# Kernel tuning notes

Hardware: AMD Instinct MI355X
Metric: run time of the kernel (lower is better)

## Reference

```python
import jax, jax.numpy as jnp
import numpy as np

B, S, H, F, K = 32, 512, 256, 256, 3
NBINS, MAX_MEL = 256, 2048


def _conv1d(x, w, b):
    # x: [B,S,Cin], w: [K,Cin,Cout] -> [B,S,Cout], padding 1 (SAME, k=3)
    return jax.lax.conv_general_dilated(x, w, (1,), 'SAME',
        dimension_numbers=('NWC', 'WIO', 'NWC')) + b


def _ln(x, g, b):
    m = jnp.mean(x, -1, keepdims=True)
    v = jnp.var(x, -1, keepdims=True)
    return (x - m) * jax.lax.rsqrt(v + 1e-5) * g + b


def _predictor(x, mask, p):
    # FastSpeech2 VariancePredictor (eval mode, dropout off)
    w1, b1, g1, be1, w2, b2, g2, be2, wl, bl = p
    h = _ln(jax.nn.relu(_conv1d(x, w1, b1)), g1, be1)
    h = _ln(jax.nn.relu(_conv1d(h, w2, b2)), g2, be2)
    out = (h @ wl + bl)[..., 0]  # [B,S]
    return jnp.where(mask, 0.0, out)  # masked_fill(mask, 0.0)


def _make_predictor_params(key, out_bias):
    ks = jax.random.split(key, 3)
    w1 = jax.random.normal(ks[0], (K, H, F), jnp.float32) * 0.03
    w2 = jax.random.normal(ks[1], (K, F, F), jnp.float32) * 0.03
    wl = jax.random.normal(ks[2], (F, 1), jnp.float32) * 0.02
    return [w1, jnp.zeros((F,), jnp.float32), jnp.ones((F,), jnp.float32), jnp.zeros((F,), jnp.float32),
            w2, jnp.zeros((F,), jnp.float32), jnp.ones((F,), jnp.float32), jnp.zeros((F,), jnp.float32),
            wl, jnp.full((1,), out_bias, jnp.float32)]


PNAMES = ['w1', 'b1', 'g1', 'be1', 'w2', 'b2', 'g2', 'be2', 'wl', 'bl']


def setup_inputs() -> dict:
    key = jax.random.key(0)
    ks = jax.random.split(key, 8)
    inp = {
        'x': jax.random.normal(ks[0], (B, S, H), jnp.float32),
        'src_mask': jnp.zeros((B, S), jnp.bool_),  # True = padded position
        'pitch_control': jnp.float32(1.0),
        'energy_control': jnp.float32(1.0),
        'duration_control': jnp.float32(1.0),
        'pitch_bins': jnp.linspace(-4.0, 4.0, NBINS - 1, dtype=jnp.float32),
        'energy_bins': jnp.linspace(-4.0, 4.0, NBINS - 1, dtype=jnp.float32),
        'pitch_emb': jax.random.normal(ks[1], (NBINS, H), jnp.float32) * 0.02,
        'energy_emb': jax.random.normal(ks[2], (NBINS, H), jnp.float32) * 0.02,
    }
    # duration predictor output bias 1.6 ~ log(5) -> avg ~4 frames/phoneme
    for i, (pref, ob) in enumerate([('dur', 1.6), ('pit', 0.0), ('ene', 0.0)]):
        for n, v in zip(PNAMES, _make_predictor_params(ks[3 + i], ob)):
            inp[pref + '_' + n] = v
    return inp


def reference(x, src_mask, pitch_control, energy_control, duration_control,
              pitch_bins, energy_bins, pitch_emb, energy_emb,
              dur_w1, dur_b1, dur_g1, dur_be1, dur_w2, dur_b2, dur_g2, dur_be2, dur_wl, dur_bl,
              pit_w1, pit_b1, pit_g1, pit_be1, pit_w2, pit_b2, pit_g2, pit_be2, pit_wl, pit_bl,
              ene_w1, ene_b1, ene_g1, ene_be1, ene_w2, ene_b2, ene_g2, ene_be2, ene_wl, ene_bl):
    dur_p = [dur_w1, dur_b1, dur_g1, dur_be1, dur_w2, dur_b2, dur_g2, dur_be2, dur_wl, dur_bl]
    pit_p = [pit_w1, pit_b1, pit_g1, pit_be1, pit_w2, pit_b2, pit_g2, pit_be2, pit_wl, pit_bl]
    ene_p = [ene_w1, ene_b1, ene_g1, ene_be1, ene_w2, ene_b2, ene_g2, ene_be2, ene_wl, ene_bl]

    log_dur = _predictor(x, src_mask, dur_p)                      # [B,S]
    pitch_pred = _predictor(x, src_mask, pit_p) * pitch_control   # inference: scaled prediction
    # torch.bucketize(v, bins) (right=False) == searchsorted side='left'
    x = x + pitch_emb[jnp.searchsorted(pitch_bins, pitch_pred, side='left')]
    energy_pred = _predictor(x, src_mask, ene_p) * energy_control
    x = x + energy_emb[jnp.searchsorted(energy_bins, energy_pred, side='left')]

    dur = jnp.maximum(jnp.round(jnp.exp(log_dur) - 1.0) * duration_control, 0.0)  # [B,S]
    dur_i = dur.astype(jnp.int32)
    mel_len = jnp.minimum(jnp.sum(dur_i, -1), MAX_MEL)            # [B]
    # Length regulator: frame t maps to phoneme idx = #{cumdur <= t}
    cum = jnp.cumsum(dur_i, 1)                                    # [B,S]
    t = jnp.arange(MAX_MEL, dtype=jnp.int32)
    idx = jax.vmap(lambda c: jnp.searchsorted(c, t, side='right'))(cum)  # [B,MAX_MEL]
    idx = jnp.clip(idx, 0, S - 1)
    x_exp = jnp.take_along_axis(x, idx[:, :, None], axis=1)       # [B,MAX_MEL,H]
    mel_mask = t[None, :] >= mel_len[:, None]                     # True = padded frame
    x_exp = jnp.where(mel_mask[:, :, None], 0.0, x_exp)
    return (x_exp, pitch_pred, energy_pred, log_dur, dur, mel_len, mel_mask)
```

## Files before the change

### kernel.cpp

```cpp
#include <hip/hip_runtime.h>
#include <stdint.h>

#define BB 32
#define SS 512
#define HH 256
#define MM (BB*SS)
#define MAXMEL 2048

typedef _Float16 f16;
typedef _Float16 f16x4 __attribute__((ext_vector_type(4)));
typedef _Float16 f16x8 __attribute__((ext_vector_type(8)));
typedef float    f32x16 __attribute__((ext_vector_type(16)));

#define BAR()  asm volatile("s_barrier" ::: "memory")
#define VMW9() asm volatile("s_waitcnt vmcnt(9)" ::: "memory")
#define VMW0() asm volatile("s_waitcnt vmcnt(0)" ::: "memory")

__device__ __forceinline__ size_t xoff(int row, int chan) {
  return ((size_t)(chan >> 4) * MM + row) * 16 + (chan & 15);
}

#define AOFF  49152
#define ABUF  12352
#define AZ    61440
#define BBUF  24576
#define LDSSZ 73856
#define WSZP ((size_t)393216)

template<int NS, int RAW>
__global__ __launch_bounds__(256) void conv16(
    const f16* __restrict__ X0h, const f16* __restrict__ X0l,
    const f16* __restrict__ X1h_, const f16* __restrict__ X1l_,
    const f16* __restrict__ W0, const f16* __restrict__ W1,
    const float* __restrict__ bias0, const float* __restrict__ bias1,
    f16* __restrict__ Y0h, f16* __restrict__ Y0l,
    f16* __restrict__ Y1h, f16* __restrict__ Y1l,
    float* __restrict__ Craw)
{
  __shared__ __align__(16) unsigned char smem[LDSSZ];
  const int tid = threadIdx.x;
  const int lane = tid & 63, wid = tid >> 6;
  const int bm = blockIdx.x, bn = blockIdx.y, bz = blockIdx.z;
  const int l31 = lane & 31, half = lane >> 5;
  const int hx4 = half << 4;
  const int wr = wid >> 1, wc = wid & 1;

  const int s0 = RAW ? bz * 8 : 0;
  const f16* Xh = (RAW || bz == 0) ? X0h : X1h_;
  const f16* Xl = (RAW || bz == 0) ? X0l : X1l_;
  const f16* Wp = (RAW || bz == 0) ? W0 : W1;

  const f16* sb[9]; int sdst[9]; int sdb[9]; size_t sstr[9];
  #pragma unroll
  for (int i = 0; i < 9; ++i) {
    int j = wid * 9 + i;
    if (j < 12) {
      int p = j / 6, seg = j % 6;
      int rowstart = bm * 128 - 32 + seg * 32;
      rowstart = rowstart < 0 ? 0 : (rowstart > MM - 32 ? MM - 32 : rowstart);
      sb[i]   = (p ? Xl : Xh) + (size_t)rowstart * 16 + lane * 8;
      sstr[i] = (size_t)MM * 16;
      sdst[i] = AOFF + p * 6144 + seg * 1024 + lane * 16;
      sdb[i]  = ABUF;
    } else {
      int jj = j - 12;
      int p = jj / 12, rest = jj % 12;
      int tap = rest >> 2, q4 = rest & 3;
      sb[i]   = Wp + (((size_t)(bn * 16) * 2 + p) * 3 + tap) * 2048
                   + q4 * 512 + lane * 8;
      sstr[i] = 12288;
      sdst[i] = p * 12288 + tap * 4096 + q4 * 1024 + lane * 16;
      sdb[i]  = BBUF;
    }
  }

  int a_addr[3][2][2];
  #pragma unroll
  for (int tap = 0; tap < 3; ++tap)
    #pragma unroll
    for (int mi = 0; mi < 2; ++mi) {
      int row_l = wr * 64 + mi * 32 + l31;
      int sseq = (bm & 3) * 128 + row_l + tap - 1;
      bool valid = (unsigned)sseq < 512u;
      int lr = row_l + tap + 31;
      #pragma unroll
      for (int p = 0; p < 2; ++p)
        a_addr[tap][mi][p] = valid ? (AOFF + p * 6144 + lr * 32) : AZ;
    }
  int b_col[2];
  #pragma unroll
  for (int n = 0; n < 2; ++n)
    b_col[n] = (wc * 64 + n * 32 + l31) * 32;

  f32x16 acc[2][2];
  #pragma unroll
  for (int mi = 0; mi < 2; ++mi)
    #pragma unroll
    for (int ni = 0; ni < 2; ++ni) acc[mi][ni] = (f32x16)0.f;

  auto STAGE = [&](int buf, int step) {
    #pragma unroll
    for (int i = 0; i < 9; ++i)
      __builtin_amdgcn_global_load_lds(
        (const __attribute__((address_space(1))) void*)(sb[i] + (size_t)step * sstr[i]),
        (__attribute__((address_space(3))) void*)(smem + sdst[i] + buf * sdb[i]),
        16, 0, 0);
  };

  auto COMP = [&](int buf) {
    #pragma unroll
    for (int tap = 0; tap < 3; ++tap) {
      f16x8 av[2][2], bv[2][2];
      #pragma unroll
      for (int p = 0; p < 2; ++p)
        #pragma unroll
        for (int q = 0; q < 2; ++q) {
          av[p][q] = *(const f16x8*)(smem + (a_addr[tap][q][p] + buf * ABUF + hx4));
          bv[p][q] = *(const f16x8*)(smem + (buf * BBUF + p * 12288 + tap * 4096 + b_col[q] + hx4));
        }
      #pragma unroll
      for (int mi = 0; mi < 2; ++mi)
        #pragma unroll
        for (int ni = 0; ni < 2; ++ni) {
          acc[mi][ni] = __builtin_amdgcn_mfma_f32_32x32x16_f16(av[0][mi], bv[0][ni], acc[mi][ni], 0, 0, 0);
          acc[mi][ni] = __builtin_amdgcn_mfma_f32_32x32x16_f16(av[0][mi], bv[1][ni], acc[mi][ni], 0, 0, 0);
          acc[mi][ni] = __builtin_amdgcn_mfma_f32_32x32x16_f16(av[1][mi], bv[0][ni], acc[mi][ni], 0, 0, 0);
        }
    }
  };

  if (tid < 4) {
    *(float4*)(smem + AZ + tid * 16) = make_float4(0.f, 0.f, 0.f, 0.f);
    *(float4*)(smem + AZ + ABUF + tid * 16) = make_float4(0.f, 0.f, 0.f, 0.f);
  }
  STAGE(0, s0); STAGE(1, s0 + 1);
  __syncthreads();

  #pragma unroll
  for (int i = 0; i < NS; ++i) {
    COMP(i & 1);
    BAR();
    if (i < NS - 2)       { STAGE(i & 1, s0 + i + 2); VMW9(); }
    else if (i == NS - 2) { VMW0(); }
    BAR();
  }

  if constexpr (RAW) {
    float* C = Craw + (size_t)bz * MM * 256;
    #pragma unroll
    for (int mi = 0; mi < 2; ++mi)
      #pragma unroll
      for (int ni = 0; ni < 2; ++ni) {
        int colg = bn * 128 + wc * 64 + ni * 32 + l31;
        #pragma unroll
        for (int r = 0; r < 16; ++r) {
          int rowl = (r & 3) + 8 * (r >> 2) + 4 * half;
          size_t rowg = (size_t)bm * 128 + wr * 64 + mi * 32 + rowl;
          C[rowg * 256 + colg] = acc[mi][ni][r];
        }
      }
  } else {
    const float* bias = bz ? bias1 : bias0;
    f16* Yh = bz ? Y1h : Y0h;
    f16* Yl = bz ? Y1l : Y0l;
    #pragma unroll
    for (int mi = 0; mi < 2; ++mi)
      #pragma unroll
      for (int ni = 0; ni < 2; ++ni) {
        int colg = bn * 128 + wc * 64 + ni * 32 + l31;
        float bvs = bias[colg];
        size_t cbase = (size_t)(colg >> 4) * MM * 16 + (colg & 15);
        #pragma unroll
        for (int r = 0; r < 16; ++r) {
          int rowl = (r & 3) + 8 * (r >> 2) + 4 * half;
          int rowg = bm * 128 + wr * 64 + mi * 32 + rowl;
          float v = fmaxf(acc[mi][ni][r] + bvs, 0.f);
          f16 h = (f16)v;
          f16 l = (f16)(v - (float)h);
          size_t o = cbase + (size_t)rowg * 16;
          Yh[o] = h;
          Yl[o] = l;
        }
      }
  }
}

__global__ __launch_bounds__(256) void wsplit6(
    const float* __restrict__ W0, const float* __restrict__ W1,
    const float* __restrict__ W2, const float* __restrict__ W3,
    const float* __restrict__ W4, const float* __restrict__ W5,
    f16* __restrict__ Wt)
{
  int z = blockIdx.y;
  const float* W = z==0?W0 : z==1?W1 : z==2?W2 : z==3?W3 : z==4?W4 : W5;
  f16* T = Wt + (size_t)z * WSZP;
  int id = blockIdx.x * 256 + threadIdx.x;
  int g = id & 1;
  int t1 = id >> 1;
  int col = t1 & 127;
  int t2 = t1 >> 7;
  int tap = t2 % 3;
  int t3 = t2 / 3;
  int p = t3 & 1;
  int t4 = t3 >> 1;
  int s = t4 & 15;
  int bn = t4 >> 4;
  int chan = s * 16 + g * 8;
  int colg = bn * 128 + col;
  f16x8 o;
  #pragma unroll
  for (int e = 0; e < 8; ++e) {
    float w = W[(size_t)(tap * 256 + chan + e) * 256 + colg];
    f16 h = (f16)w;
    o[e] = p ? (f16)(w - (float)h) : h;
  }
  *(f16x8*)(T + (size_t)id * 8) = o;
}

__global__ __launch_bounds__(256) void split2(
    const float* __restrict__ X, f16* __restrict__ Hi, f16* __restrict__ Lo)
{
  int id = blockIdx.x * 256 + threadIdx.x;
  int row = id >> 5, chan = (id & 31) * 8;
  const float* src = X + (size_t)row * 256 + chan;
  float4 v0 = *(const float4*)src;
  float4 v1 = *(const float4*)(src + 4);
  float vv[8] = {v0.x, v0.y, v0.z, v0.w, v1.x, v1.y, v1.z, v1.w};
  f16x8 h, l;
  #pragma unroll
  for (int j = 0; j < 8; ++j) {
    f16 hh = (f16)vv[j];
    h[j] = hh;
    l[j] = (f16)(vv[j] - (float)hh);
  }
  size_t o = xoff(row, chan);
  *(f16x8*)(Hi + o) = h;
  *(f16x8*)(Lo + o) = l;
}

__global__ __launch_bounds__(256) void lnF(
    f16* __restrict__ P0h, f16* __restrict__ P0l,
    f16* __restrict__ P1h, f16* __restrict__ P1l,
    const float* __restrict__ g0, const float* __restrict__ be0,
    const float* __restrict__ g1, const float* __restrict__ be1)
{
  int z = blockIdx.y;
  f16* Ph = z ? P1h : P0h;
  f16* Pl = z ? P1l : P0l;
  const float* g  = z ? g1 : g0;
  const float* be = z ? be1 : be0;
  int row  = blockIdx.x * 4 + (threadIdx.x >> 6);
  int lane = threadIdx.x & 63;
  size_t o = xoff(row, lane * 4);
  f16x4 h = *(const f16x4*)(Ph + o);
  f16x4 l = *(const f16x4*)(Pl + o);
  float v[4];
  #pragma unroll
  for (int j = 0; j < 4; ++j) v[j] = (float)h[j] + (float)l[j];
  float s = v[0] + v[1] + v[2] + v[3];
  float q = v[0]*v[0] + v[1]*v[1] + v[2]*v[2] + v[3]*v[3];
  #pragma unroll
  for (int d = 32; d > 0; d >>= 1) { s += __shfl_xor(s, d); q += __shfl_xor(q, d); }
  float mean = s * (1.f / 256.f);
  float var  = q * (1.f / 256.f) - mean * mean;
  float inv  = 1.0f / sqrtf(var + 1e-5f);
  float4 gg = *(const float4*)(g + lane * 4);
  float4 bb = *(const float4*)(be + lane * 4);
  float gv[4] = {gg.x, gg.y, gg.z, gg.w};
  float bv[4] = {bb.x, bb.y, bb.z, bb.w};
  #pragma unroll
  for (int j = 0; j < 4; ++j) {
    float oo = (v[j] - mean) * inv * gv[j] + bv[j];
    f16 hh = (f16)oo;
    h[j] = hh;
    l[j] = (f16)(oo - (float)hh);
  }
  *(f16x4*)(Ph + o) = h;
  *(f16x4*)(Pl + o) = l;
}

__global__ __launch_bounds__(256) void lnheadD(
    const f16* __restrict__ U0h, const f16* __restrict__ U0l,
    const f16* __restrict__ U1h, const f16* __restrict__ U1l,
    const float* __restrict__ g0, const float* __restrict__ be0,
    const float* __restrict__ wl0, const float* __restrict__ bl0,
    const float* __restrict__ g1, const float* __restrict__ be1,
    const float* __restrict__ wl1, const float* __restrict__ bl1,
    const unsigned char* __restrict__ mask, const float* __restrict__ pc,
    float* __restrict__ o_ldur, float* __restrict__ pred_d,
    float* __restrict__ o_pit,
    const float* __restrict__ pbins, const float* __restrict__ pemb,
    const f16* __restrict__ XPh, const f16* __restrict__ XPl,
    f16* __restrict__ X1h, f16* __restrict__ X1l)
{
  int z = blockIdx.y;
  int row  = blockIdx.x * 4 + (threadIdx.x >> 6);
  int lane = threadIdx.x & 63;
  size_t o = xoff(row, lane * 4);
  const f16* Uh = z ? U1h : U0h;
  const f16* Ul = z ? U1l : U0l;
  f16x4 h = *(const f16x4*)(Uh + o);
  f16x4 l = *(const f16x4*)(Ul + o);
  float v[4];
  #pragma unroll
  for (int j = 0; j < 4; ++j) v[j] = (float)h[j] + (float)l[j];
  float s = v[0] + v[1] + v[2] + v[3];
  float q = v[0]*v[0] + v[1]*v[1] + v[2]*v[2] + v[3]*v[3];
  #pragma unroll
  for (int d = 32; d > 0; d >>= 1) { s += __shfl_xor(s, d); q += __shfl_xor(q, d); }
  float mean = s * (1.f / 256.f);
  float var  = q * (1.f / 256.f) - mean * mean;
  float inv  = 1.0f / sqrtf(var + 1e-5f);
  const float* g  = z ? g1  : g0;
  const float* be = z ? be1 : be0;
  const float* wl = z ? wl1 : wl0;
  float4 gg = *(const float4*)(g + lane * 4);
  float4 bb = *(const float4*)(be + lane * 4);
  float4 ww = *(const float4*)(wl + lane * 4);
  float gv[4] = {gg.x, gg.y, gg.z, gg.w};
  float bv[4] = {bb.x, bb.y, bb.z, bb.w};
  float wv[4] = {ww.x, ww.y, ww.z, ww.w};
  float acc = 0.f;
  #pragma unroll
  for (int j = 0; j < 4; ++j)
    acc += ((v[j] - mean) * inv * gv[j] + bv[j]) * wv[j];
  #pragma unroll
  for (int d = 32; d > 0; d >>= 1) acc += __shfl_xor(acc, d);
  float r = acc + (z ? bl1 : bl0)[0];
  if (mask[row]) r = 0.f;
  if (z == 0) {
    if (lane == 0) { o_ldur[row] = r; pred_d[row] = r; }
  } else {
    r *= pc[0];
    if (lane == 0) o_pit[row] = r;
    int lo = 0, hi = 255;
    while (lo < hi) { int mid = (lo + hi) >> 1; if (pbins[mid] < r) lo = mid + 1; else hi = mid; }
    f16x4 xh = *(const f16x4*)(XPh + o);
    f16x4 xl = *(const f16x4*)(XPl + o);
    float4 e = *(const float4*)(pemb + (size_t)lo * HH + lane * 4);
    float ev[4] = {e.x, e.y, e.z, e.w};
    #pragma unroll
    for (int j = 0; j < 4; ++j) {
      float oo = (float)xh[j] + (float)xl[j] + ev[j];
      f16 hh = (f16)oo;
      xh[j] = hh;
      xl[j] = (f16)(oo - (float)hh);
    }
    *(f16x4*)(X1h + o) = xh;
    *(f16x4*)(X1l + o) = xl;
  }
}

__global__ __launch_bounds__(256) void lnS(
    const float* __restrict__ C0, const float* __restrict__ C1,
    const float* __restrict__ bias,
    const float* __restrict__ g, const float* __restrict__ be,
    f16* __restrict__ Yh, f16* __restrict__ Yl)
{
  int row  = blockIdx.x * 4 + (threadIdx.x >> 6);
  int lane = threadIdx.x & 63;
  size_t ci = (size_t)row * 256 + lane * 4;
  float4 a = *(const float4*)(C0 + ci);
  float4 b = *(const float4*)(C1 + ci);
  float4 bs = *(const float4*)(bias + lane * 4);
  float v[4] = {fmaxf(a.x + b.x + bs.x, 0.f), fmaxf(a.y + b.y + bs.y, 0.f),
                fmaxf(a.z + b.z + bs.z, 0.f), fmaxf(a.w + b.w + bs.w, 0.f)};
  float s = v[0] + v[1] + v[2] + v[3];
  float q = v[0]*v[0] + v[1]*v[1] + v[2]*v[2] + v[3]*v[3];
  #pragma unroll
  for (int d = 32; d > 0; d >>= 1) { s += __shfl_xor(s, d); q += __shfl_xor(q, d); }
  float mean = s * (1.f / 256.f);
  float var  = q * (1.f / 256.f) - mean * mean;
  float inv  = 1.0f / sqrtf(var + 1e-5f);
  float4 gg = *(const float4*)(g + lane * 4);
  float4 bb = *(const float4*)(be + lane * 4);
  float gv[4] = {gg.x, gg.y, gg.z, gg.w};
  float bv[4] = {bb.x, bb.y, bb.z, bb.w};
  f16x4 h, l;
  #pragma unroll
  for (int j = 0; j < 4; ++j) {
    float oo = (v[j] - mean) * inv * gv[j] + bv[j];
    f16 hh = (f16)oo;
    h[j] = hh;
    l[j] = (f16)(oo - (float)hh);
  }
  size_t o = xoff(row, lane * 4);
  *(f16x4*)(Yh + o) = h;
  *(f16x4*)(Yl + o) = l;
}

__global__ __launch_bounds__(256) void lnheadS(
    const float* __restrict__ C0, const float* __restrict__ C1,
    const float* __restrict__ bias,
    const float* __restrict__ g, const float* __restrict__ be,
    const float* __restrict__ wl, const float* __restrict__ bl,
    const unsigned char* __restrict__ mask, const float* __restrict__ ec,
    float* __restrict__ o_ene,
    const float* __restrict__ ebins, const float* __restrict__ eemb,
    const f16* __restrict__ X1h, const f16* __restrict__ X1l,
    f16* __restrict__ X2h, f16* __restrict__ X2l)
{
  int row  = blockIdx.x * 4 + (threadIdx.x >> 6);
  int lane = threadIdx.x & 63;
  size_t ci = (size_t)row * 256 + lane * 4;
  float4 a = *(const float4*)(C0 + ci);
  float4 b = *(const float4*)(C1 + ci);
  float4 bs = *(const float4*)(bias + lane * 4);
  float v[4] = {fmaxf(a.x + b.x + bs.x, 0.f), fmaxf(a.y + b.y + bs.y, 0.f),
                fmaxf(a.z + b.z + bs.z, 0.f), fmaxf(a.w + b.w + bs.w, 0.f)};
  float s = v[0] + v[1] + v[2] + v[3];
  float q = v[0]*v[0] + v[1]*v[1] + v[2]*v[2] + v[3]*v[3];
  #pragma unroll
  for (int d = 32; d > 0; d >>= 1) { s += __shfl_xor(s, d); q += __shfl_xor(q, d); }
  float mean = s * (1.f / 256.f);
  float var  = q * (1.f / 256.f) - mean * mean;
  float inv  = 1.0f / sqrtf(var + 1e-5f);
  float4 gg = *(const float4*)(g + lane * 4);
  float4 bb = *(const float4*)(be + lane * 4);
  float4 ww = *(const float4*)(wl + lane * 4);
  float gv[4] = {gg.x, gg.y, gg.z, gg.w};
  float bv[4] = {bb.x, bb.y, bb.z, bb.w};
  float wv[4] = {ww.x, ww.y, ww.z, ww.w};
  float acc = 0.f;
  #pragma unroll
  for (int j = 0; j < 4; ++j)
    acc += ((v[j] - mean) * inv * gv[j] + bv[j]) * wv[j];
  #pragma unroll
  for (int d = 32; d > 0; d >>= 1) acc += __shfl_xor(acc, d);
  float r = acc + bl[0];
  if (mask[row]) r = 0.f;
  r *= ec[0];
  if (lane == 0) o_ene[row] = r;
  int lo = 0, hi = 255;
  while (lo < hi) { int mid = (lo + hi) >> 1; if (ebins[mid] < r) lo = mid + 1; else hi = mid; }
  size_t o = xoff(row, lane * 4);
  f16x4 xh = *(const f16x4*)(X1h + o);
  f16x4 xl = *(const f16x4*)(X1l + o);
  float4 e = *(const float4*)(eemb + (size_t)lo * HH + lane * 4);
  float ev[4] = {e.x, e.y, e.z, e.w};
  #pragma unroll
  for (int j = 0; j < 4; ++j) {
    float oo = (float)xh[j] + (float)xl[j] + ev[j];
    f16 hh = (f16)oo;
    xh[j] = hh;
    xl[j] = (f16)(oo - (float)hh);
  }
  *(f16x4*)(X2h + o) = xh;
  *(f16x4*)(X2l + o) = xl;
}

__global__ __launch_bounds__(512) void dur_post(
    const float* __restrict__ logdur, const float* __restrict__ dc,
    float* __restrict__ out_dur, float* __restrict__ out_mel_len,
    int* __restrict__ cum_ws, int* __restrict__ mel_len_ws)
{
  __shared__ int wsum[8];
  int b = blockIdx.x, t = threadIdx.x;
  float ld = logdur[b * SS + t];
  float d  = fmaxf(rintf(expf(ld) - 1.f) * dc[0], 0.f);
  out_dur[b * SS + t] = d;
  int di = (int)d;
  int lane = t & 63, w = t >> 6;
  int x = di;
  #pragma unroll
  for (int dd = 1; dd < 64; dd <<= 1) {
    int n = __shfl_up(x, dd);
    if (lane >= dd) x += n;
  }
  if (lane == 63) wsum[w] = x;
  __syncthreads();
  int off = 0;
  for (int i = 0; i < w; ++i) off += wsum[i];
  x += off;
  cum_ws[b * SS + t] = x;
  if (t == SS - 1) {
    int ml = min(x, MAXMEL);
    mel_len_ws[b] = ml;
    out_mel_len[b] = (float)ml;
  }
}

__global__ __launch_bounds__(256) void gather_planes(
    const f16* __restrict__ Xhi, const f16* __restrict__ Xlo,
    const int* __restrict__ cum, const int* __restrict__ mel_len_ws,
    float* __restrict__ out_x, float* __restrict__ out_mask)
{
  __shared__ int c[SS];
  int b   = blockIdx.y;
  int tid = threadIdx.x;
  c[tid]       = cum[b * SS + tid];
  c[tid + 256] = cum[b * SS + tid + 256];
  __syncthreads();
  int w = tid >> 6, lane = tid & 63;
  int t = blockIdx.x * 4 + w;
  int lo = 0, hi = SS;
  while (lo < hi) { int mid = (lo + hi) >> 1; if (c[mid] <= t) lo = mid + 1; else hi = mid; }
  int idx = min(lo, SS - 1);
  int ml  = mel_len_ws[b];
  bool m  = (t >= ml);
  float4 v = make_float4(0.f, 0.f, 0.f, 0.f);
  if (!m) {
    size_t o = xoff(b * SS + idx, lane * 4);
    f16x4 xh = *(const f16x4*)(Xhi + o);
    f16x4 xl = *(const f16x4*)(Xlo + o);
    v.x = (float)xh[0] + (float)xl[0];
    v.y = (float)xh[1] + (float)xl[1];
    v.z = (float)xh[2] + (float)xl[2];
    v.w = (float)xh[3] + (float)xl[3];
  }
  *(float4*)(out_x + ((size_t)b * MAXMEL + t) * HH + lane * 4) = v;
  if (lane == 0) out_mask[b * MAXMEL + t] = m ? 1.f : 0.f;
}

extern "C" void kernel_launch(void* const* d_in, const int* in_sizes, int n_in,
                              void* d_out, int out_size, void* d_ws, size_t ws_size,
                              hipStream_t stream) {
  const float* x     = (const float*)d_in[0];
  const unsigned char* smask = (const unsigned char*)d_in[1];
  const float* pc    = (const float*)d_in[2];
  const float* ec    = (const float*)d_in[3];
  const float* dc    = (const float*)d_in[4];
  const float* pbins = (const float*)d_in[5];
  const float* ebins = (const float*)d_in[6];
  const float* pemb  = (const float*)d_in[7];
  const float* eemb  = (const float*)d_in[8];

  float* out = (float*)d_out;
  float* o_xexp  = out;
  float* o_pit   = out + (size_t)16777216;
  float* o_ene   = o_pit + 16384;
  float* o_ldur  = o_ene + 16384;
  float* o_dur   = o_ldur + 16384;
  float* o_mlen  = o_dur + 16384;
  float* o_mmask = o_mlen + 32;

  const size_t PL = (size_t)MM * HH;
  f16* p = (f16*)d_ws;
  f16 *XPh = p,        *XPl = p + PL;
  f16 *Tdh = p + 2*PL, *Tdl = p + 3*PL;
  f16 *Tph = p + 4*PL, *Tpl = p + 5*PL;
  f16 *Udh = p + 6*PL, *Udl = p + 7*PL;
  f16 *Uph = p + 8*PL, *Upl = p + 9*PL;
  f16 *X1h = p + 10*PL, *X1l = p + 11*PL;
  f16 *Teh = p + 12*PL, *Tel = p + 13*PL;
  f16 *X2h = p + 14*PL, *X2l = p + 15*PL;
  f16* Wt  = p + 16*PL;
  float* C0 = (float*)(Wt + 6 * WSZP);
  float* C1 = C0 + (size_t)MM * 256;
  float* pred_d = C1 + (size_t)MM * 256;
  int*   cum = (int*)(pred_d + MM);
  int*   mlw = cum + MM;

  #define WPK(i) (Wt + (size_t)(i) * WSZP)

  wsplit6<<<dim3(192, 6), 256, 0, stream>>>(
      (const float*)d_in[9], (const float*)d_in[13], (const float*)d_in[19],
      (const float*)d_in[23], (const float*)d_in[29], (const float*)d_in[33], Wt);

  split2<<<2048, 256, 0, stream>>>(x, XPh, XPl);

  dim3 cgrid(128, 2, 2);
  dim3 rgrid(MM / 4);
  dim3 rgrid2(MM / 4, 2);

  conv16<16, 0><<<cgrid, 256, 0, stream>>>(
      XPh, XPl, XPh, XPl, WPK(0), WPK(2),
      (const float*)d_in[10], (const float*)d_in[20],
      Tdh, Tdl, Tph, Tpl, nullptr);
  lnF<<<rgrid2, 256, 0, stream>>>(Tdh, Tdl, Tph, Tpl,
      (const float*)d_in[11], (const float*)d_in[12],
      (const float*)d_in[21], (const float*)d_in[22]);
  conv16<16, 0><<<cgrid, 256, 0, stream>>>(
      Tdh, Tdl, Tph, Tpl, WPK(1), WPK(3),
      (const float*)d_in[14], (const float*)d_in[24],
      Udh, Udl, Uph, Upl, nullptr);
  lnheadD<<<rgrid2, 256, 0, stream>>>(
      Udh, Udl, Uph, Upl,
      (const float*)d_in[15], (const float*)d_in[16],
      (const float*)d_in[17], (const float*)d_in[18],
      (const float*)d_in[25], (const float*)d_in[26],
      (const float*)d_in[27], (const float*)d_in[28],
      smask, pc, o_ldur, pred_d, o_pit, pbins, pemb,
      XPh, XPl, X1h, X1l);
  dur_post<<<BB, 512, 0, stream>>>(pred_d, dc, o_dur, o_mlen, cum, mlw);

  conv16<8, 1><<<cgrid, 256, 0, stream>>>(
      X1h, X1l, X1h, X1l, WPK(4), WPK(4),
      nullptr, nullptr, nullptr, nullptr, nullptr, nullptr, C0);
  lnS<<<rgrid, 256, 0, stream>>>(C0, C1, (const float*)d_in[30],
      (const float*)d_in[31], (const float*)d_in[32], Teh, Tel);
  conv16<8, 1><<<cgrid, 256, 0, stream>>>(
      Teh, Tel, Teh, Tel, WPK(5), WPK(5),
      nullptr, nullptr, nullptr, nullptr, nullptr, nullptr, C0);
  lnheadS<<<rgrid, 256, 0, stream>>>(C0, C1, (const float*)d_in[34],
      (const float*)d_in[35], (const float*)d_in[36],
      (const float*)d_in[37], (const float*)d_in[38],
      smask, ec, o_ene, ebins, eemb, X1h, X1l, X2h, X2l);

  dim3 ggrid(MAXMEL / 4, BB);
  gather_planes<<<ggrid, 256, 0, stream>>>(X2h, X2l, cum, mlw, o_xexp, o_mmask);

  #undef WPK
}
```

Baseline: 228.1 us.

## Switch activation planes to 8-channel panes and widen row kernels to 8 channels/lane

Changes the fp16 hi/lo activation layout from 16-channel panes to 8-channel panes, so each row occupies one 16-byte chunk per pane. The conv kernel's LDS staging and MFMA operand addressing, the weight packing, and all layernorm, head and gather kernels are updated to match. Those row kernels now process two rows per wave with 8 channels per lane and 16-byte vector loads and stores, halving their grid sizes. The goal is wider global accesses and possibly fewer LDS bank conflicts in the conv, at the cost of a different LDS access pattern that could conflict differently.

```diff
diff --git a/kernel.cpp b/kernel.cpp
--- a/kernel.cpp
+++ b/kernel.cpp
@@ -16,8 +16,8 @@
 #define VMW9() asm volatile("s_waitcnt vmcnt(9)" ::: "memory")
 #define VMW0() asm volatile("s_waitcnt vmcnt(0)" ::: "memory")
 
-__device__ __forceinline__ size_t xoff(int row, int chan) {
-  return ((size_t)(chan >> 4) * MM + row) * 16 + (chan & 15);
+__device__ __forceinline__ size_t xoff8(int pane, int row) {
+  return ((size_t)pane * MM + row) * 8;
 }
 
 #define AOFF  49152
@@ -42,7 +42,6 @@
   const int lane = tid & 63, wid = tid >> 6;
   const int bm = blockIdx.x, bn = blockIdx.y, bz = blockIdx.z;
   const int l31 = lane & 31, half = lane >> 5;
-  const int hx4 = half << 4;
   const int wr = wid >> 1, wc = wid & 1;
 
   const int s0 = RAW ? bz * 8 : 0;
@@ -55,21 +54,23 @@
   for (int i = 0; i < 9; ++i) {
     int j = wid * 9 + i;
     if (j < 12) {
-      int p = j / 6, seg = j % 6;
-      int rowstart = bm * 128 - 32 + seg * 32;
-      rowstart = rowstart < 0 ? 0 : (rowstart > MM - 32 ? MM - 32 : rowstart);
-      sb[i]   = (p ? Xl : Xh) + (size_t)rowstart * 16 + lane * 8;
+      int p = j / 6, rem = j % 6, g = rem / 3, seg = rem % 3;
+      int lr = seg * 64 + lane;
+      int row = bm * 128 - 32 + lr;
+      row = row < 0 ? 0 : (row >= MM ? MM - 1 : row);
+      sb[i]   = (p ? Xl : Xh) + ((size_t)g * MM + row) * 8;
       sstr[i] = (size_t)MM * 16;
-      sdst[i] = AOFF + p * 6144 + seg * 1024 + lane * 16;
+      sdst[i] = AOFF + p * 6144 + g * 3072 + lr * 16;
       sdb[i]  = ABUF;
     } else {
       int jj = j - 12;
       int p = jj / 12, rest = jj % 12;
-      int tap = rest >> 2, q4 = rest & 3;
-      sb[i]   = Wp + (((size_t)(bn * 16) * 2 + p) * 3 + tap) * 2048
-                   + q4 * 512 + lane * 8;
+      int tap = rest >> 2, q = rest & 3;
+      int g = q >> 1, h2 = q & 1;
+      sb[i]   = Wp + ((((((size_t)(bn * 16) * 2 + p) * 3 + tap) * 2 + g) * 128)
+                      + h2 * 64 + lane) * 8;
       sstr[i] = 12288;
-      sdst[i] = p * 12288 + tap * 4096 + q4 * 1024 + lane * 16;
+      sdst[i] = p * 12288 + tap * 4096 + g * 2048 + h2 * 1024 + lane * 16;
       sdb[i]  = BBUF;
     }
   }
@@ -85,12 +86,13 @@
       int lr = row_l + tap + 31;
       #pragma unroll
       for (int p = 0; p < 2; ++p)
-        a_addr[tap][mi][p] = valid ? (AOFF + p * 6144 + lr * 32) : AZ;
+        a_addr[tap][mi][p] = valid ? (AOFF + p * 6144 + half * 3072 + lr * 16)
+                                   : AZ;
     }
-  int b_col[2];
+  int b_base[2];
   #pragma unroll
   for (int n = 0; n < 2; ++n)
-    b_col[n] = (wc * 64 + n * 32 + l31) * 32;
+    b_base[n] = half * 2048 + (wc * 64 + n * 32 + l31) * 16;
 
   f32x16 acc[2][2];
   #pragma unroll
@@ -115,8 +117,8 @@
       for (int p = 0; p < 2; ++p)
         #pragma unroll
         for (int q = 0; q < 2; ++q) {
-          av[p][q] = *(const f16x8*)(smem + (a_addr[tap][q][p] + buf * ABUF + hx4));
-          bv[p][q] = *(const f16x8*)(smem + (buf * BBUF + p * 12288 + tap * 4096 + b_col[q] + hx4));
+          av[p][q] = *(const f16x8*)(smem + (a_addr[tap][q][p] + buf * ABUF));
+          bv[p][q] = *(const f16x8*)(smem + (buf * BBUF + p * 12288 + tap * 4096 + b_base[q]));
         }
       #pragma unroll
       for (int mi = 0; mi < 2; ++mi)
@@ -169,7 +171,7 @@
       for (int ni = 0; ni < 2; ++ni) {
         int colg = bn * 128 + wc * 64 + ni * 32 + l31;
         float bvs = bias[colg];
-        size_t cbase = (size_t)(colg >> 4) * MM * 16 + (colg & 15);
+        size_t cbase = (size_t)(colg >> 3) * MM * 8 + (colg & 7);
         #pragma unroll
         for (int r = 0; r < 16; ++r) {
           int rowl = (r & 3) + 8 * (r >> 2) + 4 * half;
@@ -177,7 +179,7 @@
           float v = fmaxf(acc[mi][ni][r] + bvs, 0.f);
           f16 h = (f16)v;
           f16 l = (f16)(v - (float)h);
-          size_t o = cbase + (size_t)rowg * 16;
+          size_t o = cbase + (size_t)rowg * 8;
           Yh[o] = h;
           Yl[o] = l;
         }
@@ -195,16 +197,13 @@
   const float* W = z==0?W0 : z==1?W1 : z==2?W2 : z==3?W3 : z==4?W4 : W5;
   f16* T = Wt + (size_t)z * WSZP;
   int id = blockIdx.x * 256 + threadIdx.x;
-  int g = id & 1;
-  int t1 = id >> 1;
-  int col = t1 & 127;
-  int t2 = t1 >> 7;
-  int tap = t2 % 3;
-  int t3 = t2 / 3;
-  int p = t3 & 1;
-  int t4 = t3 >> 1;
-  int s = t4 & 15;
-  int bn = t4 >> 4;
+  int col = id & 127;
+  int t = id >> 7;
+  int g = t & 1; t >>= 1;
+  int tap = t % 3; t /= 3;
+  int p = t & 1; t >>= 1;
+  int s = t & 15;
+  int bn = t >> 4;
   int chan = s * 16 + g * 8;
   int colg = bn * 128 + col;
   f16x8 o;
@@ -221,8 +220,8 @@
     const float* __restrict__ X, f16* __restrict__ Hi, f16* __restrict__ Lo)
 {
   int id = blockIdx.x * 256 + threadIdx.x;
-  int row = id >> 5, chan = (id & 31) * 8;
-  const float* src = X + (size_t)row * 256 + chan;
+  int row = id >> 5, pane = id & 31;
+  const float* src = X + (size_t)row * 256 + pane * 8;
   float4 v0 = *(const float4*)src;
   float4 v1 = *(const float4*)(src + 4);
   float vv[8] = {v0.x, v0.y, v0.z, v0.w, v1.x, v1.y, v1.z, v1.w};
@@ -233,10 +232,11 @@
     h[j] = hh;
     l[j] = (f16)(vv[j] - (float)hh);
   }
-  size_t o = xoff(row, chan);
+  size_t o = xoff8(pane, row);
   *(f16x8*)(Hi + o) = h;
   *(f16x8*)(Lo + o) = l;
 }
+
 
 __global__ __launch_bounds__(256) void lnF(
     f16* __restrict__ P0h, f16* __restrict__ P0l,
@@ -249,34 +249,38 @@
   f16* Pl = z ? P1l : P0l;
   const float* g  = z ? g1 : g0;
   const float* be = z ? be1 : be0;
-  int row  = blockIdx.x * 4 + (threadIdx.x >> 6);
-  int lane = threadIdx.x & 63;
-  size_t o = xoff(row, lane * 4);
-  f16x4 h = *(const f16x4*)(Ph + o);
-  f16x4 l = *(const f16x4*)(Pl + o);
-  float v[4];
-  #pragma unroll
-  for (int j = 0; j < 4; ++j) v[j] = (float)h[j] + (float)l[j];
-  float s = v[0] + v[1] + v[2] + v[3];
-  float q = v[0]*v[0] + v[1]*v[1] + v[2]*v[2] + v[3]*v[3];
-  #pragma unroll
-  for (int d = 32; d > 0; d >>= 1) { s += __shfl_xor(s, d); q += __shfl_xor(q, d); }
+  int tid = threadIdx.x, lane = tid & 63;
+  int row  = blockIdx.x * 8 + (tid >> 6) * 2 + (lane >> 5);
+  int pane = lane & 31;
+  size_t o = xoff8(pane, row);
+  f16x8 h = *(const f16x8*)(Ph + o);
+  f16x8 l = *(const f16x8*)(Pl + o);
+  float v[8];
+  #pragma unroll
+  for (int j = 0; j < 8; ++j) v[j] = (float)h[j] + (float)l[j];
+  float s = 0.f, q = 0.f;
+  #pragma unroll
+  for (int j = 0; j < 8; ++j) { s += v[j]; q += v[j] * v[j]; }
+  #pragma unroll
+  for (int d = 16; d > 0; d >>= 1) { s += __shfl_xor(s, d); q += __shfl_xor(q, d); }
   float mean = s * (1.f / 256.f);
   float var  = q * (1.f / 256.f) - mean * mean;
   float inv  = 1.0f / sqrtf(var + 1e-5f);
-  float4 gg = *(const float4*)(g + lane * 4);
-  float4 bb = *(const float4*)(be + lane * 4);
-  float gv[4] = {gg.x, gg.y, gg.z, gg.w};
-  float bv[4] = {bb.x, bb.y, bb.z, bb.w};
-  #pragma unroll
-  for (int j = 0; j < 4; ++j) {
+  float4 ga = *(const float4*)(g + pane * 8);
+  float4 gb = *(const float4*)(g + pane * 8 + 4);
+  float4 ba = *(const float4*)(be + pane * 8);
+  float4 bb = *(const float4*)(be + pane * 8 + 4);
+  float gv[8] = {ga.x, ga.y, ga.z, ga.w, gb.x, gb.y, gb.z, gb.w};
+  float bv[8] = {ba.x, ba.y, ba.z, ba.w, bb.x, bb.y, bb.z, bb.w};
+  #pragma unroll
+  for (int j = 0; j < 8; ++j) {
     float oo = (v[j] - mean) * inv * gv[j] + bv[j];
     f16 hh = (f16)oo;
     h[j] = hh;
     l[j] = (f16)(oo - (float)hh);
   }
-  *(f16x4*)(Ph + o) = h;
-  *(f16x4*)(Pl + o) = l;
+  *(f16x8*)(Ph + o) = h;
+  *(f16x8*)(Pl + o) = l;
 }
 
 __global__ __launch_bounds__(256) void lnheadD(
@@ -294,60 +298,66 @@
     f16* __restrict__ X1h, f16* __restrict__ X1l)
 {
   int z = blockIdx.y;
-  int row  = blockIdx.x * 4 + (threadIdx.x >> 6);
-  int lane = threadIdx.x & 63;
-  size_t o = xoff(row, lane * 4);
+  int tid = threadIdx.x, lane = tid & 63;
+  int row  = blockIdx.x * 8 + (tid >> 6) * 2 + (lane >> 5);
+  int pane = lane & 31;
+  size_t o = xoff8(pane, row);
   const f16* Uh = z ? U1h : U0h;
   const f16* Ul = z ? U1l : U0l;
-  f16x4 h = *(const f16x4*)(Uh + o);
-  f16x4 l = *(const f16x4*)(Ul + o);
-  float v[4];
-  #pragma unroll
-  for (int j = 0; j < 4; ++j) v[j] = (float)h[j] + (float)l[j];
-  float s = v[0] + v[1] + v[2] + v[3];
-  float q = v[0]*v[0] + v[1]*v[1] + v[2]*v[2] + v[3]*v[3];
-  #pragma unroll
-  for (int d = 32; d > 0; d >>= 1) { s += __shfl_xor(s, d); q += __shfl_xor(q, d); }
+  f16x8 h = *(const f16x8*)(Uh + o);
+  f16x8 l = *(const f16x8*)(Ul + o);
+  float v[8];
+  #pragma unroll
+  for (int j = 0; j < 8; ++j) v[j] = (float)h[j] + (float)l[j];
+  float s = 0.f, q = 0.f;
+  #pragma unroll
+  for (int j = 0; j < 8; ++j) { s += v[j]; q += v[j] * v[j]; }
+  #pragma unroll
+  for (int d = 16; d > 0; d >>= 1) { s += __shfl_xor(s, d); q += __shfl_xor(q, d); }
   float mean = s * (1.f / 256.f);
   float var  = q * (1.f / 256.f) - mean * mean;
   float inv  = 1.0f / sqrtf(var + 1e-5f);
   const float* g  = z ? g1  : g0;
   const float* be = z ? be1 : be0;
   const float* wl = z ? wl1 : wl0;
-  float4 gg = *(const float4*)(g + lane * 4);
-  float4 bb = *(const float4*)(be + lane * 4);
-  float4 ww = *(const float4*)(wl + lane * 4);
-  float gv[4] = {gg.x, gg.y, gg.z, gg.w};
-  float bv[4] = {bb.x, bb.y, bb.z, bb.w};
-  float wv[4] = {ww.x, ww.y, ww.z, ww.w};
+  float4 ga = *(const float4*)(g + pane * 8);
+  float4 gb = *(const float4*)(g + pane * 8 + 4);
+  float4 ba = *(const float4*)(be + pane * 8);
+  float4 bb = *(const float4*)(be + pane * 8 + 4);
+  float4 wa = *(const float4*)(wl + pane * 8);
+  float4 wb = *(const float4*)(wl + pane * 8 + 4);
+  float gv[8] = {ga.x, ga.y, ga.z, ga.w, gb.x, gb.y, gb.z, gb.w};
+  float bv[8] = {ba.x, ba.y, ba.z, ba.w, bb.x, bb.y, bb.z, bb.w};
+  float wv[8] = {wa.x, wa.y, wa.z, wa.w, wb.x, wb.y, wb.z, wb.w};
   float acc = 0.f;
   #pragma unroll
-  for (int j = 0; j < 4; ++j)
+  for (int j = 0; j < 8; ++j)
     acc += ((v[j] - mean) * inv * gv[j] + bv[j]) * wv[j];
   #pragma unroll
-  for (int d = 32; d > 0; d >>= 1) acc += __shfl_xor(acc, d);
+  for (int d = 16; d > 0; d >>= 1) acc += __shfl_xor(acc, d);
   float r = acc + (z ? bl1 : bl0)[0];
   if (mask[row]) r = 0.f;
   if (z == 0) {
-    if (lane == 0) { o_ldur[row] = r; pred_d[row] = r; }
+    if (pane == 0) { o_ldur[row] = r; pred_d[row] = r; }
   } else {
     r *= pc[0];
-    if (lane == 0) o_pit[row] = r;
+    if (pane == 0) o_pit[row] = r;
     int lo = 0, hi = 255;
     while (lo < hi) { int mid = (lo + hi) >> 1; if (pbins[mid] < r) lo = mid + 1; else hi = mid; }
-    f16x4 xh = *(const f16x4*)(XPh + o);
-    f16x4 xl = *(const f16x4*)(XPl + o);
-    float4 e = *(const float4*)(pemb + (size_t)lo * HH + lane * 4);
-    float ev[4] = {e.x, e.y, e.z, e.w};
-    #pragma unroll
-    for (int j = 0; j < 4; ++j) {
+    f16x8 xh = *(const f16x8*)(XPh + o);
+    f16x8 xl = *(const f16x8*)(XPl + o);
+    float4 ea = *(const float4*)(pemb + (size_t)lo * HH + pane * 8);
+    float4 eb = *(const float4*)(pemb + (size_t)lo * HH + pane * 8 + 4);
+    float ev[8] = {ea.x, ea.y, ea.z, ea.w, eb.x, eb.y, eb.z, eb.w};
+    #pragma unroll
+    for (int j = 0; j < 8; ++j) {
       float oo = (float)xh[j] + (float)xl[j] + ev[j];
       f16 hh = (f16)oo;
       xh[j] = hh;
       xl[j] = (f16)(oo - (float)hh);
     }
-    *(f16x4*)(X1h + o) = xh;
-    *(f16x4*)(X1l + o) = xl;
+    *(f16x8*)(X1h + o) = xh;
+    *(f16x8*)(X1l + o) = xl;
   }
 }
 
@@ -357,36 +367,45 @@
     const float* __restrict__ g, const float* __restrict__ be,
     f16* __restrict__ Yh, f16* __restrict__ Yl)
 {
-  int row  = blockIdx.x * 4 + (threadIdx.x >> 6);
-  int lane = threadIdx.x & 63;
-  size_t ci = (size_t)row * 256 + lane * 4;
-  float4 a = *(const float4*)(C0 + ci);
-  float4 b = *(const float4*)(C1 + ci);
-  float4 bs = *(const float4*)(bias + lane * 4);
-  float v[4] = {fmaxf(a.x + b.x + bs.x, 0.f), fmaxf(a.y + b.y + bs.y, 0.f),
-                fmaxf(a.z + b.z + bs.z, 0.f), fmaxf(a.w + b.w + bs.w, 0.f)};
-  float s = v[0] + v[1] + v[2] + v[3];
-  float q = v[0]*v[0] + v[1]*v[1] + v[2]*v[2] + v[3]*v[3];
-  #pragma unroll
-  for (int d = 32; d > 0; d >>= 1) { s += __shfl_xor(s, d); q += __shfl_xor(q, d); }
+  int tid = threadIdx.x, lane = tid & 63;
+  int row  = blockIdx.x * 8 + (tid >> 6) * 2 + (lane >> 5);
+  int pane = lane & 31;
+  size_t ci = (size_t)row * 256 + pane * 8;
+  float4 a0 = *(const float4*)(C0 + ci);
+  float4 a1 = *(const float4*)(C0 + ci + 4);
+  float4 b0 = *(const float4*)(C1 + ci);
+  float4 b1 = *(const float4*)(C1 + ci + 4);
+  float4 s0 = *(const float4*)(bias + pane * 8);
+  float4 s1 = *(const float4*)(bias + pane * 8 + 4);
+  float v[8] = {fmaxf(a0.x + b0.x + s0.x, 0.f), fmaxf(a0.y + b0.y + s0.y, 0.f),
+                fmaxf(a0.z + b0.z + s0.z, 0.f), fmaxf(a0.w + b0.w + s0.w, 0.f),
+                fmaxf(a1.x + b1.x + s1.x, 0.f), fmaxf(a1.y + b1.y + s1.y, 0.f),
+                fmaxf(a1.z + b1.z + s1.z, 0.f), fmaxf(a1.w + b1.w + s1.w, 0.f)};
+  float s = 0.f, q = 0.f;
+  #pragma unroll
+  for (int j = 0; j < 8; ++j) { s += v[j]; q += v[j] * v[j]; }
+  #pragma unroll
+  for (int d = 16; d > 0; d >>= 1) { s += __shfl_xor(s, d); q += __shfl_xor(q, d); }
   float mean = s * (1.f / 256.f);
   float var  = q * (1.f / 256.f) - mean * mean;
   float inv  = 1.0f / sqrtf(var + 1e-5f);
-  float4 gg = *(const float4*)(g + lane * 4);
-  float4 bb = *(const float4*)(be + lane * 4);
-  float gv[4] = {gg.x, gg.y, gg.z, gg.w};
-  float bv[4] = {bb.x, bb.y, bb.z, bb.w};
-  f16x4 h, l;
-  #pragma unroll
-  for (int j = 0; j < 4; ++j) {
+  float4 ga = *(const float4*)(g + pane * 8);
+  float4 gb = *(const float4*)(g + pane * 8 + 4);
+  float4 ba = *(const float4*)(be + pane * 8);
+  float4 bb = *(const float4*)(be + pane * 8 + 4);
+  float gv[8] = {ga.x, ga.y, ga.z, ga.w, gb.x, gb.y, gb.z, gb.w};
+  float bv[8] = {ba.x, ba.y, ba.z, ba.w, bb.x, bb.y, bb.z, bb.w};
+  f16x8 h, l;
+  #pragma unroll
+  for (int j = 0; j < 8; ++j) {
     float oo = (v[j] - mean) * inv * gv[j] + bv[j];
     f16 hh = (f16)oo;
     h[j] = hh;
     l[j] = (f16)(oo - (float)hh);
   }
-  size_t o = xoff(row, lane * 4);
-  *(f16x4*)(Yh + o) = h;
-  *(f16x4*)(Yl + o) = l;
+  size_t o = xoff8(pane, row);
+  *(f16x8*)(Yh + o) = h;
+  *(f16x8*)(Yl + o) = l;
 }
 
 __global__ __launch_bounds__(256) void lnheadS(
@@ -400,53 +419,64 @@
     const f16* __restrict__ X1h, const f16* __restrict__ X1l,
     f16* __restrict__ X2h, f16* __restrict__ X2l)
 {
-  int row  = blockIdx.x * 4 + (threadIdx.x >> 6);
-  int lane = threadIdx.x & 63;
-  size_t ci = (size_t)row * 256 + lane * 4;
-  float4 a = *(const float4*)(C0 + ci);
-  float4 b = *(const float4*)(C1 + ci);
-  float4 bs = *(const float4*)(bias + lane * 4);
-  float v[4] = {fmaxf(a.x + b.x + bs.x, 0.f), fmaxf(a.y + b.y + bs.y, 0.f),
-                fmaxf(a.z + b.z + bs.z, 0.f), fmaxf(a.w + b.w + bs.w, 0.f)};
-  float s = v[0] + v[1] + v[2] + v[3];
-  float q = v[0]*v[0] + v[1]*v[1] + v[2]*v[2] + v[3]*v[3];
-  #pragma unroll
-  for (int d = 32; d > 0; d >>= 1) { s += __shfl_xor(s, d); q += __shfl_xor(q, d); }
+  int tid = threadIdx.x, lane = tid & 63;
+  int row  = blockIdx.x * 8 + (tid >> 6) * 2 + (lane >> 5);
+  int pane = lane & 31;
+  size_t ci = (size_t)row * 256 + pane * 8;
+  float4 a0 = *(const float4*)(C0 + ci);
+  float4 a1 = *(const float4*)(C0 + ci + 4);
+  float4 b0 = *(const float4*)(C1 + ci);
+  float4 b1 = *(const float4*)(C1 + ci + 4);
+  float4 s0 = *(const float4*)(bias + pane * 8);
+  float4 s1 = *(const float4*)(bias + pane * 8 + 4);
+  float v[8] = {fmaxf(a0.x + b0.x + s0.x, 0.f), fmaxf(a0.y + b0.y + s0.y, 0.f),
+                fmaxf(a0.z + b0.z + s0.z, 0.f), fmaxf(a0.w + b0.w + s0.w, 0.f),
+                fmaxf(a1.x + b1.x + s1.x, 0.f), fmaxf(a1.y + b1.y + s1.y, 0.f),
+                fmaxf(a1.z + b1.z + s1.z, 0.f), fmaxf(a1.w + b1.w + s1.w, 0.f)};
+  float s = 0.f, q = 0.f;
+  #pragma unroll
+  for (int j = 0; j < 8; ++j) { s += v[j]; q += v[j] * v[j]; }
+  #pragma unroll
+  for (int d = 16; d > 0; d >>= 1) { s += __shfl_xor(s, d); q += __shfl_xor(q, d); }
   float mean = s * (1.f / 256.f);
   float var  = q * (1.f / 256.f) - mean * mean;
   float inv  = 1.0f / sqrtf(var + 1e-5f);
-  float4 gg = *(const float4*)(g + lane * 4);
-  float4 bb = *(const float4*)(be + lane * 4);
-  float4 ww = *(const float4*)(wl + lane * 4);
-  float gv[4] = {gg.x, gg.y, gg.z, gg.w};
-  float bv[4] = {bb.x, bb.y, bb.z, bb.w};
-  float wv[4] = {ww.x, ww.y, ww.z, ww.w};
+  float4 ga = *(const float4*)(g + pane * 8);
+  float4 gb = *(const float4*)(g + pane * 8 + 4);
+  float4 ba = *(const float4*)(be + pane * 8);
+  float4 bb = *(const float4*)(be + pane * 8 + 4);
+  float4 wa = *(const float4*)(wl + pane * 8);
+  float4 wb = *(const float4*)(wl + pane * 8 + 4);
+  float gv[8] = {ga.x, ga.y, ga.z, ga.w, gb.x, gb.y, gb.z, gb.w};
+  float bv[8] = {ba.x, ba.y, ba.z, ba.w, bb.x, bb.y, bb.z, bb.w};
+  float wv[8] = {wa.x, wa.y, wa.z, wa.w, wb.x, wb.y, wb.z, wb.w};
   float acc = 0.f;
   #pragma unroll
-  for (int j = 0; j < 4; ++j)
+  for (int j = 0; j < 8; ++j)
     acc += ((v[j] - mean) * inv * gv[j] + bv[j]) * wv[j];
   #pragma unroll
-  for (int d = 32; d > 0; d >>= 1) acc += __shfl_xor(acc, d);
+  for (int d = 16; d > 0; d >>= 1) acc += __shfl_xor(acc, d);
   float r = acc + bl[0];
   if (mask[row]) r = 0.f;
   r *= ec[0];
-  if (lane == 0) o_ene[row] = r;
+  if (pane == 0) o_ene[row] = r;
   int lo = 0, hi = 255;
   while (lo < hi) { int mid = (lo + hi) >> 1; if (ebins[mid] < r) lo = mid + 1; else hi = mid; }
-  size_t o = xoff(row, lane * 4);
-  f16x4 xh = *(const f16x4*)(X1h + o);
-  f16x4 xl = *(const f16x4*)(X1l + o);
-  float4 e = *(const float4*)(eemb + (size_t)lo * HH + lane * 4);
-  float ev[4] = {e.x, e.y, e.z, e.w};
-  #pragma unroll
-  for (int j = 0; j < 4; ++j) {
+  size_t o = xoff8(pane, row);
+  f16x8 xh = *(const f16x8*)(X1h + o);
+  f16x8 xl = *(const f16x8*)(X1l + o);
+  float4 ea = *(const float4*)(eemb + (size_t)lo * HH + pane * 8);
+  float4 eb = *(const float4*)(eemb + (size_t)lo * HH + pane * 8 + 4);
+  float ev[8] = {ea.x, ea.y, ea.z, ea.w, eb.x, eb.y, eb.z, eb.w};
+  #pragma unroll
+  for (int j = 0; j < 8; ++j) {
     float oo = (float)xh[j] + (float)xl[j] + ev[j];
     f16 hh = (f16)oo;
     xh[j] = hh;
     xl[j] = (f16)(oo - (float)hh);
   }
-  *(f16x4*)(X2h + o) = xh;
-  *(f16x4*)(X2l + o) = xl;
+  *(f16x8*)(X2h + o) = xh;
+  *(f16x8*)(X2l + o) = xl;
 }
 
 __global__ __launch_bounds__(512) void dur_post(
@@ -491,25 +521,26 @@
   c[tid]       = cum[b * SS + tid];
   c[tid + 256] = cum[b * SS + tid + 256];
   __syncthreads();
-  int w = tid >> 6, lane = tid & 63;
-  int t = blockIdx.x * 4 + w;
+  int lane = tid & 63, w = tid >> 6;
+  int t = blockIdx.x * 8 + w * 2 + (lane >> 5);
+  int pane = lane & 31;
   int lo = 0, hi = SS;
   while (lo < hi) { int mid = (lo + hi) >> 1; if (c[mid] <= t) lo = mid + 1; else hi = mid; }
   int idx = min(lo, SS - 1);
   int ml  = mel_len_ws[b];
   bool m  = (t >= ml);
-  float4 v = make_float4(0.f, 0.f, 0.f, 0.f);
+  float v[8] = {0.f, 0.f, 0.f, 0.f, 0.f, 0.f, 0.f, 0.f};
   if (!m) {
-    size_t o = xoff(b * SS + idx, lane * 4);
-    f16x4 xh = *(const f16x4*)(Xhi + o);
-    f16x4 xl = *(const f16x4*)(Xlo + o);
-    v.x = (float)xh[0] + (float)xl[0];
-    v.y = (float)xh[1] + (float)xl[1];
-    v.z = (float)xh[2] + (float)xl[2];
-    v.w = (float)xh[3] + (float)xl[3];
-  }
-  *(float4*)(out_x + ((size_t)b * MAXMEL + t) * HH + lane * 4) = v;
-  if (lane == 0) out_mask[b * MAXMEL + t] = m ? 1.f : 0.f;
+    size_t o = xoff8(pane, b * SS + idx);
+    f16x8 xh = *(const f16x8*)(Xhi + o);
+    f16x8 xl = *(const f16x8*)(Xlo + o);
+    #pragma unroll
+    for (int j = 0; j < 8; ++j) v[j] = (float)xh[j] + (float)xl[j];
+  }
+  float* dst = out_x + ((size_t)b * MAXMEL + t) * HH + pane * 8;
+  *(float4*)dst       = make_float4(v[0], v[1], v[2], v[3]);
+  *(float4*)(dst + 4) = make_float4(v[4], v[5], v[6], v[7]);
+  if (pane == 0) out_mask[b * MAXMEL + t] = m ? 1.f : 0.f;
 }
 
 extern "C" void kernel_launch(void* const* d_in, const int* in_sizes, int n_in,
@@ -560,21 +591,21 @@
   split2<<<2048, 256, 0, stream>>>(x, XPh, XPl);
 
   dim3 cgrid(128, 2, 2);
-  dim3 rgrid(MM / 4);
-  dim3 rgrid2(MM / 4, 2);
+  dim3 rgrid8(MM / 8);
+  dim3 rgrid8x2(MM / 8, 2);
 
   conv16<16, 0><<<cgrid, 256, 0, stream>>>(
       XPh, XPl, XPh, XPl, WPK(0), WPK(2),
       (const float*)d_in[10], (const float*)d_in[20],
       Tdh, Tdl, Tph, Tpl, nullptr);
-  lnF<<<rgrid2, 256, 0, stream>>>(Tdh, Tdl, Tph, Tpl,
+  lnF<<<rgrid8x2, 256, 0, stream>>>(Tdh, Tdl, Tph, Tpl,
       (const float*)d_in[11], (const float*)d_in[12],
       (const float*)d_in[21], (const float*)d_in[22]);
   conv16<16, 0><<<cgrid, 256, 0, stream>>>(
       Tdh, Tdl, Tph, Tpl, WPK(1), WPK(3),
       (const float*)d_in[14], (const float*)d_in[24],
       Udh, Udl, Uph, Upl, nullptr);
-  lnheadD<<<rgrid2, 256, 0, stream>>>(
+  lnheadD<<<rgrid8x2, 256, 0, stream>>>(
       Udh, Udl, Uph, Upl,
       (const float*)d_in[15], (const float*)d_in[16],
       (const float*)d_in[17], (const float*)d_in[18],
@@ -587,17 +618,17 @@
   conv16<8, 1><<<cgrid, 256, 0, stream>>>(
       X1h, X1l, X1h, X1l, WPK(4), WPK(4),
       nullptr, nullptr, nullptr, nullptr, nullptr, nullptr, C0);
-  lnS<<<rgrid, 256, 0, stream>>>(C0, C1, (const float*)d_in[30],
+  lnS<<<rgrid8, 256, 0, stream>>>(C0, C1, (const float*)d_in[30],
       (const float*)d_in[31], (const float*)d_in[32], Teh, Tel);
   conv16<8, 1><<<cgrid, 256, 0, stream>>>(
       Teh, Tel, Teh, Tel, WPK(5), WPK(5),
       nullptr, nullptr, nullptr, nullptr, nullptr, nullptr, C0);
-  lnheadS<<<rgrid, 256, 0, stream>>>(C0, C1, (const float*)d_in[34],
+  lnheadS<<<rgrid8, 256, 0, stream>>>(C0, C1, (const float*)d_in[34],
       (const float*)d_in[35], (const float*)d_in[36],
       (const float*)d_in[37], (const float*)d_in[38],
       smask, ec, o_ene, ebins, eemb, X1h, X1l, X2h, X2l);
 
-  dim3 ggrid(MAXMEL / 4, BB);
+  dim3 ggrid(MAXMEL / 8, BB);
   gather_planes<<<ggrid, 256, 0, stream>>>(X2h, X2l, cum, mlw, o_xexp, o_mmask);
 
   #undef WPK
```

Measured after the change: 233.0 us (median of 2 runs). +2.1%, slower.
